# Performance work log

Measured on AMD Instinct MI355X. Metric: run time of the kernel, lower is better.

Reference implementation:

```python
import jax, jax.numpy as jnp
import numpy as np
from functools import partial

WIDTH = 2560
LRU = 2560
HEADS = 8
DCONV = 4
B = 4
L = 2048


def setup_inputs() -> dict:
    key = jax.random.key(0)
    ks = jax.random.split(key, 16)
    bw = LRU // HEADS
    x = jax.random.normal(ks[0], (B, L, WIDTH), dtype=jnp.float32)
    segment_pos = jnp.broadcast_to(jnp.arange(L, dtype=jnp.int32), (B, L))
    # indices of the last DCONV frames of the left-padded conv input (length L+DCONV-1)
    base = (jnp.arange(DCONV, dtype=jnp.int32) + (L - 1))
    conv_idx = jnp.broadcast_to(base, (B, LRU, DCONV))
    s = 0.02
    return {
        "x": x,
        "segment_pos": segment_pos,
        "conv_idx": conv_idx,
        "Wx": jax.random.normal(ks[1], (LRU, WIDTH), jnp.float32) * s,
        "bx": jax.random.normal(ks[2], (LRU,), jnp.float32) * s,
        "Wy": jax.random.normal(ks[3], (LRU, WIDTH), jnp.float32) * s,
        "conv_w": jax.random.normal(ks[4], (LRU, DCONV), jnp.float32) * s,  # depthwise kernel
        "conv_b": jax.random.normal(ks[5], (LRU,), jnp.float32) * s,
        "gx_w": jax.random.normal(ks[6], (HEADS, bw, bw), jnp.float32) * s,
        "gx_b": jax.random.normal(ks[7], (HEADS, bw), jnp.float32) * s,
        "ga_w": jax.random.normal(ks[8], (HEADS, bw, bw), jnp.float32) * s,
        "ga_b": jax.random.normal(ks[9], (HEADS, bw), jnp.float32) * s,
        "a_param": jax.random.normal(ks[10], (LRU,), jnp.float32),
        "y_bias": jax.random.normal(ks[11], (1, 1, LRU), jnp.float32) * s,
        "Wout": jax.random.normal(ks[12], (WIDTH, LRU), jnp.float32) * s,
        "bout": jax.random.normal(ks[13], (WIDTH,), jnp.float32) * s,
    }


def _block_diag(x, w):
    # x: [B,L,(h*i)], w: [h,i,j] -> [B,L,(h*j)]
    b, l, _ = x.shape
    h, bw, _ = w.shape
    xb = x.reshape(b, l, h, bw)
    y = jnp.einsum('blhi,hij->blhj', xb, w)
    return y.reshape(b, l, h * bw)


def _scan_op(c1, c2):
    a1, b1 = c1
    a2, b2 = c2
    return (a1 * a2, a2 * b1 + b2)


def reference(x, segment_pos, conv_idx, Wx, bx, Wy, conv_w, conv_b,
              gx_w, gx_b, ga_w, ga_b, a_param, y_bias, Wout, bout):
    dc = conv_w.shape[1]
    seqlen = x.shape[1]

    y = jnp.einsum('bld,ed->ble', x, Wy)                 # linear_y (no bias)
    xl = jnp.einsum('bld,ed->ble', x, Wx) + bx           # linear_x

    # causal depthwise conv1d, padding dc-1 on the left, keep first seqlen
    xpad = jnp.pad(xl, ((0, 0), (dc - 1, 0), (0, 0)))    # [B, L+dc-1, LRU]
    xc = conv_b + sum(conv_w[:, k] * xpad[:, k:k + seqlen, :] for k in range(dc))

    # conv_state: gather of padded (channels-first) input at conv_idx
    conv_state = jnp.take_along_axis(xpad.transpose(0, 2, 1), conv_idx.astype(jnp.int32), axis=2)

    gx = _block_diag(xc, gx_w)  # fuse_bias=True: bias added inside rg_lru
    ga = _block_diag(xc, ga_w)

    # rg_lru_ref
    reset = (segment_pos == 0).astype(x.dtype)[..., None]        # [B,L,1]
    gate_x = jax.nn.sigmoid(gx + gx_b.reshape(-1))
    gate_a = jax.nn.sigmoid(ga + ga_b.reshape(-1))
    c = -8.0 * jax.nn.softplus(a_param)
    log_a = c * gate_a
    a = jnp.exp(log_a) * (1.0 - reset)
    multiplier = jnp.sqrt(1.0 - jnp.exp(2.0 * log_a))
    multiplier = reset + (1.0 - reset) * multiplier
    normalized_x = xc * gate_x * multiplier

    _, h = jax.lax.associative_scan(_scan_op, (a, normalized_x), axis=1)
    last_h = h[:, -1]

    out = h * jax.nn.gelu(y + y_bias, approximate=False)
    out = jnp.einsum('ble,de->bld', out, Wout) + bout    # linear_out
    return out, conv_state, last_h
```

## Files before the change

### kernel.cpp

```cpp
#include <hip/hip_runtime.h>
#include <hip/hip_bf16.h>

#define WIDTH_ 2560
#define LRU_   2560
#define HEADS_ 8
#define BW_    320
#define DCONV_ 4
#define BB     4
#define LL     2048
#define MROWS  (BB*LL)
#define NCH    32
#define CLEN   (LL/NCH)

typedef unsigned short ushort_t;
typedef __attribute__((ext_vector_type(8))) short short8;
typedef __attribute__((ext_vector_type(4))) float f32x4;

__device__ __forceinline__ unsigned short f2bf(float f) {
  union { float f; unsigned u; } v; v.f = f;
  unsigned r = v.u + 0x7fffu + ((v.u >> 16) & 1u);
  return (unsigned short)(r >> 16);
}
__device__ __forceinline__ float bf2f(unsigned short h) {
  union { unsigned u; float f; } v; v.u = ((unsigned)h) << 16;
  return v.f;
}
__device__ __forceinline__ void async_load16(const void* g, void* l) {
  __builtin_amdgcn_global_load_lds(
      (const __attribute__((address_space(1))) unsigned*)g,
      (__attribute__((address_space(3))) unsigned*)l, 16, 0, 0);
}
__device__ __forceinline__ float sigmoidf_(float x) {
  return 1.f / (1.f + __expf(-x));
}
__device__ __forceinline__ size_t pkaddr(int e, int m, int PL) {
  return ((size_t)(e >> 3) * PL + m) * 8 + (e & 7);
}

__global__ void tp_pack(const float* __restrict__ src, ushort_t* __restrict__ dst,
                        int R, int C, int PL, int RO) {
  __shared__ float tile[64][65];
  const int r0 = blockIdx.x * 64, c0 = blockIdx.y * 64;
  const int t = threadIdx.x;
#pragma unroll
  for (int it = 0; it < 4; ++it) {
    int row = it * 16 + (t >> 4);
    int col = (t & 15) * 4;
    *(float4*)&tile[row][col] = *(const float4*)&src[(size_t)(r0 + row) * C + c0 + col];
  }
  __syncthreads();
#pragma unroll
  for (int it = 0; it < 2; ++it) {
    int c8 = it * 4 + (t >> 6);
    int m  = t & 63;
    ushort_t o[8];
#pragma unroll
    for (int j = 0; j < 8; ++j) o[j] = f2bf(tile[m][c8 * 8 + j]);
    *(short8*)&dst[((size_t)(c0 / 8 + c8) * PL + RO + r0 + m) * 8] = *(short8*)o;
  }
}

__global__ void gw_pack(const float* __restrict__ w, ushort_t* __restrict__ dst,
                        int RO, int n_) {
  int i = blockIdx.x * blockDim.x + threadIdx.x;
  if (i >= n_) return;
  int n = i % BW_;
  int k = (i / BW_) % BW_;
  int h = i / (BW_ * BW_);
  dst[((size_t)(h * 40 + (k >> 3)) * 640 + RO + n) * 8 + (k & 7)] =
      f2bf(w[((size_t)h * BW_ + k) * BW_ + n]);
}

__global__ void ctab_kernel(const float* __restrict__ apar, float* __restrict__ ctab) {
  int e = blockIdx.x * blockDim.x + threadIdx.x;
  if (e >= LRU_) return;
  float ap = apar[e];
  float sp = (ap > 15.f) ? ap : log1pf(expf(ap));
  ctab[e] = -8.f * sp;
}


#define STG_A(KT, H, BUF) do { \
  _Pragma("unroll") for (int u_ = 0; u_ < 2; ++u_) \
    async_load16(Ach + aoff[u_] + (size_t)(KT) * aKt + (H) * 2048, \
                 smem + ((BUF) * 2 + (H)) * 16384 + ldst[u_]); } while (0)
#define STG_B(KT, H, BUF) do { \
  _Pragma("unroll") for (int u_ = 0; u_ < 2; ++u_) \
    async_load16(Bch + boff[u_] + (size_t)(KT) * bKt + (H) * 2048, \
                 smem + 65536 + ((BUF) * 2 + (H)) * 16384 + ldst[u_]); } while (0)

#define PHASE(BUF, Q, STAGE_STMT, VMN) do { \
  __builtin_amdgcn_sched_barrier(0); \
  const char* Ah_ = smem + ((BUF) * 2 + wr) * 16384; \
  const char* Bh_ = smem + 65536 + ((BUF) * 2 + (wc >> 1)) * 16384; \
  if ((Q) == 0) { \
    _Pragma("unroll") for (int nf = 0; nf < 4; ++nf) \
      _Pragma("unroll") for (int s = 0; s < 2; ++s) \
        bfr[nf][s] = *(const short8*)(Bh_ + ((s * 4 + l4) * 128 + brow + nf * 16 + l15) * 16); \
  } \
  short8 a_[2][2]; \
  _Pragma("unroll") for (int mm = 0; mm < 2; ++mm) \
    _Pragma("unroll") for (int s = 0; s < 2; ++s) \
      a_[mm][s] = *(const short8*)(Ah_ + ((s * 4 + l4) * 128 + ((Q) * 2 + mm) * 16 + l15) * 16); \
  STAGE_STMT; \
  __builtin_amdgcn_sched_barrier(0); \
  __builtin_amdgcn_s_barrier(); \
  asm volatile("s_waitcnt lgkmcnt(0)" ::: "memory"); \
  __builtin_amdgcn_sched_barrier(0); \
  __builtin_amdgcn_s_setprio(1); \
  _Pragma("unroll") for (int mm = 0; mm < 2; ++mm) \
    _Pragma("unroll") for (int nf = 0; nf < 4; ++nf) \
      _Pragma("unroll") for (int s = 0; s < 2; ++s) \
        acc[(Q) * 2 + mm][nf] = __builtin_amdgcn_mfma_f32_16x16x32_bf16( \
            a_[mm][s], bfr[nf][s], acc[(Q) * 2 + mm][nf], 0, 0, 0); \
  __builtin_amdgcn_s_setprio(0); \
  if ((VMN) == 4)      asm volatile("s_waitcnt vmcnt(4)" ::: "memory"); \
  else if ((VMN) == 0) asm volatile("s_waitcnt vmcnt(0)" ::: "memory"); \
  __builtin_amdgcn_sched_barrier(0); \
  __builtin_amdgcn_s_barrier(); \
} while (0)

template<int EPI>
__global__ __launch_bounds__(512, 2)
void gemm_pk(const ushort_t* __restrict__ A,
             const ushort_t* __restrict__ B, int NPL,
             void* __restrict__ C0, void* __restrict__ C1,
             const float* __restrict__ bias) {
  __shared__ char smem[131072];
  const int tid = threadIdx.x;
  const int lane = tid & 63, w = tid >> 6;
  const int wr = w >> 2, wc = w & 3;
  const int l15 = lane & 15, l4 = lane >> 4;
  const int brow = (wc & 1) * 64;

  const int nblk = gridDim.x;
  const int TN = nblk >> 5;
  const int x8 = blockIdx.x & 7, c = blockIdx.x >> 3;
  const int tm = (x8 * 4 + c / TN) * 256;
  const int tn = (c % TN) * 256;

  const char* Ach = (const char*)A;
  const char* Bch = (const char*)B;
  const size_t aKt = (size_t)8 * MROWS * 16;
  const size_t bKt = (size_t)8 * NPL * 16;

  size_t aoff[2], boff[2]; int ldst[2];
#pragma unroll
  for (int u = 0; u < 2; ++u) {
    int lb = (u * 512 + tid) * 16;
    int slot = lb >> 11, m = (lb >> 4) & 127;
    aoff[u] = ((size_t)slot * MROWS + tm + m) * 16;
    boff[u] = ((size_t)slot * NPL + tn + m) * 16;
    ldst[u] = lb;
  }

  f32x4 acc[8][4] = {};
  short8 bfr[4][2];

  STG_B(0, 0, 0); STG_B(0, 1, 0); STG_A(0, 0, 0); STG_A(0, 1, 0);
  STG_B(1, 0, 1); STG_B(1, 1, 1);
  asm volatile("s_waitcnt vmcnt(4)" ::: "memory");
  __builtin_amdgcn_sched_barrier(0);
  __builtin_amdgcn_s_barrier();

#pragma unroll 1
  for (int i = 0; i < 20; ++i) {
    const int k1 = 2 * i + 1, k2 = 2 * i + 2, k3 = 2 * i + 3;
    const bool v2 = (k2 < 40), v3 = (k3 < 40);
    PHASE(0, 0, STG_A(k1, 0, 1), -1);
    PHASE(0, 1, STG_A(k1, 1, 1), -1);
    PHASE(0, 2, if (v2) STG_B(k2, 0, 0), -1);
    PHASE(0, 3, if (v2) STG_B(k2, 1, 0), (v2 ? 4 : 0));
    PHASE(1, 0, if (v2) STG_A(k2, 0, 0), -1);
    PHASE(1, 1, if (v2) STG_A(k2, 1, 0), -1);
    PHASE(1, 2, if (v3) STG_B(k3, 0, 1), -1);
    PHASE(1, 3, if (v3) STG_B(k3, 1, 1), (v3 ? 4 : (v2 ? 0 : -1)));
  }

  const int crow0 = tm + wr * 128 + l4 * 4;
  const int ccol0 = tn + wc * 64 + l15;
#pragma unroll
  for (int m = 0; m < 8; ++m)
#pragma unroll
    for (int n = 0; n < 4; ++n) {
      const int col = ccol0 + n * 16;
#pragma unroll
      for (int r = 0; r < 4; ++r) {
        const int row = crow0 + m * 16 + r;
        float v = acc[m][n][r];
        if (EPI == 0) {
          ((float*)C0)[(size_t)row * 2560 + col] = v + bias[col];
        } else {
          if (col < 2560)
            ((ushort_t*)C0)[pkaddr(col, row, MROWS)] = f2bf(v + bias[col]);
          else
            ((ushort_t*)C1)[pkaddr(col - 2560, row, MROWS)] = f2bf(v);
        }
      }
    }
}

__global__ __launch_bounds__(256, 2)
void gate_gemm(const ushort_t* __restrict__ A,
               const ushort_t* __restrict__ Bw,
               ushort_t* __restrict__ GX,
               ushort_t* __restrict__ AAo,
               const float* __restrict__ gxb, const float* __restrict__ gab,
               const float* __restrict__ ctab, const int* __restrict__ seg) {
  constexpr int BM = 128, NF = 2;
  __shared__ char smem[24576];
  const int tid = threadIdx.x;
  const int w = tid >> 6, lane = tid & 63;
  const int wr = w >> 1, wc = w & 1;
  const int l15 = lane & 15, l4 = lane >> 4;
  const int tm = blockIdx.x * BM;
  const int tn = blockIdx.y * 64;
  const int z = blockIdx.z;

  const char* aS[2]; int lda_[2];
#pragma unroll
  for (int u = 0; u < 2; ++u) {
    int lb = (u * 256 + tid) * 16;
    int slot = lb >> 11, m = (lb >> 4) & 127;
    aS[u] = (const char*)A + ((size_t)(z * 40 + slot) * MROWS + tm + m) * 16;
    lda_[u] = lb;
  }
  const char* bS; int ldb_;
  {
    int lb = tid * 16;
    int slot = lb >> 10, n = (lb >> 4) & 63;
    bS = (const char*)Bw + ((size_t)(z * 40 + slot) * 640 + tn + n) * 16;
    ldb_ = 8192 + lb;
  }
  const size_t aStep = (size_t)4 * MROWS * 16;
  const size_t bStep = (size_t)4 * 640 * 16;

#define GSTG(KT, BUF) do { \
  _Pragma("unroll") for (int u_ = 0; u_ < 2; ++u_) \
    async_load16(aS[u_] + (size_t)(KT) * aStep, smem + (BUF) * 12288 + lda_[u_]); \
  async_load16(bS + (size_t)(KT) * bStep, smem + (BUF) * 12288 + ldb_); \
} while (0)

  f32x4 acc[4][NF] = {};
  const int aRd = l4 * 2048 + (wr * 64 + l15) * 16;
  const int bRd = 8192 + l4 * 1024 + (wc * 32 + l15) * 16;

  GSTG(0, 0);
#pragma unroll 1
  for (int kt = 0; kt < 10; ++kt) {
    const int p = kt & 1;
    if (kt < 9) {
      GSTG(kt + 1, p ^ 1);
      asm volatile("s_waitcnt vmcnt(3)" ::: "memory");
    } else {
      asm volatile("s_waitcnt vmcnt(0)" ::: "memory");
    }
    __builtin_amdgcn_sched_barrier(0);
    __builtin_amdgcn_s_barrier();
    const char* buf = smem + p * 12288;
    short8 af[4], bfr[NF];
#pragma unroll
    for (int mf = 0; mf < 4; ++mf)
      af[mf] = *(const short8*)(buf + aRd + mf * 256);
#pragma unroll
    for (int nf = 0; nf < NF; ++nf)
      bfr[nf] = *(const short8*)(buf + bRd + nf * 256);
#pragma unroll
    for (int mf = 0; mf < 4; ++mf)
#pragma unroll
      for (int nf = 0; nf < NF; ++nf)
        acc[mf][nf] = __builtin_amdgcn_mfma_f32_16x16x32_bf16(af[mf], bfr[nf], acc[mf][nf], 0, 0, 0);
    __builtin_amdgcn_sched_barrier(0);
    __builtin_amdgcn_s_barrier();
  }
#undef GSTG

  const int crow0 = tm + wr * 64 + l4 * 4;
  const int ccol0 = tn + wc * 32 + l15;
#pragma unroll
  for (int mf = 0; mf < 4; ++mf) {
#pragma unroll
    for (int nf = 0; nf < NF; ++nf) {
      const int cih = ccol0 + nf * 16;
#pragma unroll
      for (int r = 0; r < 4; ++r) {
        const int row = crow0 + mf * 16 + r;
        if (cih < BW_) {
          const int gc = z * BW_ + cih;
          float v = acc[mf][nf][r] + gxb[gc];
          float xc = bf2f(A[pkaddr(gc, row, MROWS)]);
          GX[pkaddr(gc, row, MROWS)] = f2bf(xc * sigmoidf_(v));
        } else {
          const int gc = z * BW_ + cih - BW_;
          float v = acc[mf][nf][r] + gab[gc];
          float la = ctab[gc] * sigmoidf_(v);
          float av = (seg[row] == 0) ? 0.f : expf(la);
          AAo[pkaddr(gc, row, MROWS)] = f2bf(av);
        }
      }
    }
  }
}

__global__ void conv_pk(const ushort_t* __restrict__ xl, const float* __restrict__ convw,
                        const float* __restrict__ convb, ushort_t* __restrict__ xc) {
  int i = blockIdx.x * blockDim.x + threadIdx.x;
  if (i >= 320 * MROWS) return;
  int m = i % MROWS;
  int p = i / MROWS;
  int t = m % LL;
  const ushort_t* pl = xl + (size_t)p * MROWS * 8;
  short8 v0 = {}, v1 = {}, v2 = {}, v3;
  v3 = *(const short8*)(pl + (size_t)m * 8);
  if (t >= 1) v2 = *(const short8*)(pl + (size_t)(m - 1) * 8);
  if (t >= 2) v1 = *(const short8*)(pl + (size_t)(m - 2) * 8);
  if (t >= 3) v0 = *(const short8*)(pl + (size_t)(m - 3) * 8);
  ushort_t o[8];
#pragma unroll
  for (int u = 0; u < 8; ++u) {
    int e = p * 8 + u;
    float4 wv = ((const float4*)convw)[e];
    float acc = convb[e];
    acc += wv.x * bf2f((ushort_t)v0[u]);
    acc += wv.y * bf2f((ushort_t)v1[u]);
    acc += wv.z * bf2f((ushort_t)v2[u]);
    acc += wv.w * bf2f((ushort_t)v3[u]);
    o[u] = f2bf(acc);
  }
  *(short8*)(xc + (size_t)p * MROWS * 8 + (size_t)m * 8) = *(short8*)o;
}

__global__ void conv_state_kernel(const ushort_t* __restrict__ xl, const int* __restrict__ cidx,
                                  float* __restrict__ cs) {
  int i = blockIdx.x * blockDim.x + threadIdx.x;
  if (i >= BB * LRU_ * DCONV_) return;
  int e = (i / DCONV_) % LRU_;
  int b = i / (DCONV_ * LRU_);
  int idx = cidx[i];
  int ts = idx - (DCONV_ - 1);
  float v = 0.f;
  if (ts >= 0 && ts < LL) v = bf2f(xl[pkaddr(e, b * LL + ts, MROWS)]);
  cs[i] = v;
}

__global__ void scanA(const ushort_t* __restrict__ AA, const ushort_t* __restrict__ GX,
                      float* __restrict__ cA, float* __restrict__ cH) {
  int i = blockIdx.x * blockDim.x + threadIdx.x;
  if (i >= BB * NCH * LRU_) return;
  int e = i % LRU_;
  int c = (i / LRU_) % NCH;
  int b = i / (LRU_ * NCH);
  float Ap = 1.f, h = 0.f;
  size_t base = pkaddr(e, b * LL + c * CLEN, MROWS);
  for (int t = 0; t < CLEN; ++t) {
    size_t j = base + (size_t)t * 8;
    float a = bf2f(AA[j]);
    float nx = bf2f(GX[j]) * sqrtf(fmaxf(0.f, 1.f - a * a));
    Ap *= a;
    h = a * h + nx;
  }
  cA[i] = Ap; cH[i] = h;
}

__global__ void scanB(const float* __restrict__ cA, const float* __restrict__ cH,
                      float* __restrict__ hInit) {
  int i = blockIdx.x * blockDim.x + threadIdx.x;
  if (i >= BB * LRU_) return;
  int e = i % LRU_;
  int b = i / LRU_;
  float h = 0.f;
  for (int c = 0; c < NCH; ++c) {
    size_t j = ((size_t)b * NCH + c) * LRU_ + e;
    hInit[j] = h;
    h = cA[j] * h + cH[j];
  }
}

__global__ void scanC(const ushort_t* __restrict__ AA, const ushort_t* __restrict__ GXpre,
                      const float* __restrict__ hInit, const ushort_t* __restrict__ ybf,
                      const float* __restrict__ ybias, float* __restrict__ lastH) {
  int i = blockIdx.x * blockDim.x + threadIdx.x;
  if (i >= BB * NCH * LRU_) return;
  int e = i % LRU_;
  int c = (i / LRU_) % NCH;
  int b = i / (LRU_ * NCH);
  float h = hInit[i];
  float yb = ybias[e];
  ushort_t* pre = (ushort_t*)GXpre;
  size_t base = pkaddr(e, b * LL + c * CLEN, MROWS);
  for (int t = 0; t < CLEN; ++t) {
    size_t j = base + (size_t)t * 8;
    float a = bf2f(AA[j]);
    float nx = bf2f(GXpre[j]) * sqrtf(fmaxf(0.f, 1.f - a * a));
    h = a * h + nx;
    float yv = bf2f(ybf[j]) + yb;
    float g = 0.5f * yv * (1.f + erff(yv * 0.70710678118f));
    pre[j] = f2bf(h * g);
  }
  if (c == NCH - 1) lastH[(size_t)b * LRU_ + e] = h;
}

extern "C" void kernel_launch(void* const* d_in, const int* in_sizes, int n_in,
                              void* d_out, int out_size, void* d_ws, size_t ws_size,
                              hipStream_t stream) {
  const float* x     = (const float*)d_in[0];
  const int*   seg   = (const int*)d_in[1];
  const int*   cidx  = (const int*)d_in[2];
  const float* Wx    = (const float*)d_in[3];
  const float* bx    = (const float*)d_in[4];
  const float* Wy    = (const float*)d_in[5];
  const float* convw = (const float*)d_in[6];
  const float* convb = (const float*)d_in[7];
  const float* gxw   = (const float*)d_in[8];
  const float* gxb   = (const float*)d_in[9];
  const float* gaw   = (const float*)d_in[10];
  const float* gab   = (const float*)d_in[11];
  const float* apar  = (const float*)d_in[12];
  const float* ybias = (const float*)d_in[13];
  const float* Wout  = (const float*)d_in[14];
  const float* bout  = (const float*)d_in[15];

  float* out    = (float*)d_out;
  float* cs_out = out + (size_t)MROWS * WIDTH_;
  float* lh_out = cs_out + (size_t)BB * LRU_ * DCONV_;

  ushort_t* ybf = (ushort_t*)d_out;
  ushort_t* AA  = (ushort_t*)((char*)d_out + (size_t)41943040);

  const size_t SZ_BIG = (size_t)MROWS * LRU_ * 2;
  const size_t SZ_WC  = (size_t)(2 * LRU_) * WIDTH_ * 2;
  const size_t SZ_GW  = (size_t)HEADS_ * 640 * BW_ * 2;
  const size_t SZ_SM  = (size_t)BB * NCH * LRU_ * 4;
  size_t need = SZ_BIG * 3 + SZ_WC + SZ_GW + 10240 + SZ_SM * 3;
  if (ws_size < need) return;

  char* p = (char*)d_ws;
  ushort_t* xpk   = (ushort_t*)p; p += SZ_BIG;
  ushort_t* wpk   = (ushort_t*)p; p += SZ_WC;
  ushort_t* T2    = (ushort_t*)p; p += SZ_BIG;
  ushort_t* xcbf  = (ushort_t*)p; p += SZ_BIG;
  ushort_t* gwT   = (ushort_t*)p; p += SZ_GW;
  float*    ctab  = (float*)p;    p += 10240;
  float*    cA    = (float*)p;    p += SZ_SM;
  float*    cH    = (float*)p;    p += SZ_SM;
  float*    hInit = (float*)p;    p += SZ_SM;
  ushort_t* woutpk = wpk;

  const int BLK = 256;
  tp_pack<<<dim3(MROWS / 64, WIDTH_ / 64), 256, 0, stream>>>(x, xpk, MROWS, WIDTH_, MROWS, 0);
  tp_pack<<<dim3(LRU_ / 64, WIDTH_ / 64), 256, 0, stream>>>(Wx, wpk, LRU_, WIDTH_, 2 * LRU_, 0);
  tp_pack<<<dim3(LRU_ / 64, WIDTH_ / 64), 256, 0, stream>>>(Wy, wpk, LRU_, WIDTH_, 2 * LRU_, LRU_);

  gemm_pk<1><<<640, 512, 0, stream>>>(xpk, wpk, 2 * LRU_, T2, ybf, bx);

  tp_pack<<<dim3(LRU_ / 64, WIDTH_ / 64), 256, 0, stream>>>(Wout, woutpk, WIDTH_, LRU_, WIDTH_, 0);

  conv_pk<<<(320 * MROWS + BLK - 1) / BLK, BLK, 0, stream>>>(T2, convw, convb, xcbf);
  conv_state_kernel<<<(BB * LRU_ * DCONV_ + BLK - 1) / BLK, BLK, 0, stream>>>(T2, cidx, cs_out);

  gw_pack<<<(HEADS_ * BW_ * BW_ + BLK - 1) / BLK, BLK, 0, stream>>>(gxw, gwT, 0, HEADS_ * BW_ * BW_);
  gw_pack<<<(HEADS_ * BW_ * BW_ + BLK - 1) / BLK, BLK, 0, stream>>>(gaw, gwT, BW_, HEADS_ * BW_ * BW_);
  ctab_kernel<<<(LRU_ + BLK - 1) / BLK, BLK, 0, stream>>>(apar, ctab);

  gate_gemm<<<dim3(MROWS / 128, 10, HEADS_), BLK, 0, stream>>>(
      xcbf, gwT, T2, AA, gxb, gab, ctab, seg);

  scanA<<<(BB * NCH * LRU_ + BLK - 1) / BLK, BLK, 0, stream>>>(AA, T2, cA, cH);
  scanB<<<(BB * LRU_ + BLK - 1) / BLK, BLK, 0, stream>>>(cA, cH, hInit);
  scanC<<<(BB * NCH * LRU_ + BLK - 1) / BLK, BLK, 0, stream>>>(AA, T2, hInit, ybf, ybias, lh_out);

  gemm_pk<0><<<320, 512, 0, stream>>>(T2, woutpk, WIDTH_, out, nullptr, bout);
}
```

Before: 579.0 us.

## Keep full A row-tile resident in LDS for gate GEMM; fuse GELU into projection epilogue

The gate GEMM is restructured so each block loads its entire 128-row by 320-channel xc tile into LDS once and streams all 20 output column slices of the head's weights through a double buffer. Previously A was re-read for each of 10 column tiles, and xc was re-read from global memory in the epilogue. The GELU on y+bias moves into the first GEMM's epilogue, so the scan reads a precomputed gate and skips erf work inside the serial loop. The cost is 120KB of LDS per block, which lowers occupancy, along with a smaller grid of 512 blocks and erf evaluation in the GEMM epilogue.

Result: slower. 743.1 us (+28.3%).

```diff
diff --git a/kernel.cpp b/kernel.cpp
--- a/kernel.cpp
+++ b/kernel.cpp
@@ -125,7 +125,7 @@
 void gemm_pk(const ushort_t* __restrict__ A,
              const ushort_t* __restrict__ B, int NPL,
              void* __restrict__ C0, void* __restrict__ C1,
-             const float* __restrict__ bias) {
+             const float* __restrict__ bias, const float* __restrict__ ybias) {
   __shared__ char smem[131072];
   const int tid = threadIdx.x;
   const int lane = tid & 63, w = tid >> 6;
@@ -191,10 +191,13 @@
         if (EPI == 0) {
           ((float*)C0)[(size_t)row * 2560 + col] = v + bias[col];
         } else {
-          if (col < 2560)
+          if (col < 2560) {
             ((ushort_t*)C0)[pkaddr(col, row, MROWS)] = f2bf(v + bias[col]);
-          else
-            ((ushort_t*)C1)[pkaddr(col - 2560, row, MROWS)] = f2bf(v);
+          } else {
+            float yv = v + ybias[col - 2560];
+            float g = 0.5f * yv * (1.f + erff(yv * 0.70710678118f));
+            ((ushort_t*)C1)[pkaddr(col - 2560, row, MROWS)] = f2bf(g);
+          }
         }
       }
     }
@@ -207,99 +210,90 @@
                ushort_t* __restrict__ AAo,
                const float* __restrict__ gxb, const float* __restrict__ gab,
                const float* __restrict__ ctab, const int* __restrict__ seg) {
-  constexpr int BM = 128, NF = 2;
-  __shared__ char smem[24576];
+  __shared__ char smem[122880];
   const int tid = threadIdx.x;
-  const int w = tid >> 6, lane = tid & 63;
-  const int wr = w >> 1, wc = w & 1;
+  const int lane = tid & 63, w = tid >> 6;
   const int l15 = lane & 15, l4 = lane >> 4;
-  const int tm = blockIdx.x * BM;
-  const int tn = blockIdx.y * 64;
-  const int z = blockIdx.z;
-
-  const char* aS[2]; int lda_[2];
-#pragma unroll
-  for (int u = 0; u < 2; ++u) {
+  const int tm = blockIdx.x * 128;
+  const int z = blockIdx.y;
+
+#pragma unroll
+  for (int u = 0; u < 20; ++u) {
     int lb = (u * 256 + tid) * 16;
     int slot = lb >> 11, m = (lb >> 4) & 127;
-    aS[u] = (const char*)A + ((size_t)(z * 40 + slot) * MROWS + tm + m) * 16;
-    lda_[u] = lb;
-  }
-  const char* bS; int ldb_;
-  {
-    int lb = tid * 16;
-    int slot = lb >> 10, n = (lb >> 4) & 63;
-    bS = (const char*)Bw + ((size_t)(z * 40 + slot) * 640 + tn + n) * 16;
-    ldb_ = 8192 + lb;
-  }
-  const size_t aStep = (size_t)4 * MROWS * 16;
-  const size_t bStep = (size_t)4 * 640 * 16;
-
-#define GSTG(KT, BUF) do { \
-  _Pragma("unroll") for (int u_ = 0; u_ < 2; ++u_) \
-    async_load16(aS[u_] + (size_t)(KT) * aStep, smem + (BUF) * 12288 + lda_[u_]); \
-  async_load16(bS + (size_t)(KT) * bStep, smem + (BUF) * 12288 + ldb_); \
-} while (0)
-
-  f32x4 acc[4][NF] = {};
-  const int aRd = l4 * 2048 + (wr * 64 + l15) * 16;
-  const int bRd = 8192 + l4 * 1024 + (wc * 32 + l15) * 16;
-
-  GSTG(0, 0);
+    async_load16((const char*)A + ((size_t)(z * 40 + slot) * MROWS + tm + m) * 16,
+                 smem + lb);
+  }
+#define GSTG_B(S, BUF) do { \
+  _Pragma("unroll") for (int u_ = 0; u_ < 5; ++u_) { \
+    int lb_ = (u_ * 256 + tid) * 16; \
+    int slot_ = lb_ >> 9, n_ = (lb_ >> 4) & 31; \
+    async_load16((const char*)Bw + ((size_t)(z * 40 + slot_) * 640 + (S) * 32 + n_) * 16, \
+                 smem + 81920 + (BUF) * 20480 + lb_); \
+  } } while (0)
+
+  GSTG_B(0, 0);
+
 #pragma unroll 1
-  for (int kt = 0; kt < 10; ++kt) {
-    const int p = kt & 1;
-    if (kt < 9) {
-      GSTG(kt + 1, p ^ 1);
-      asm volatile("s_waitcnt vmcnt(3)" ::: "memory");
+  for (int s = 0; s < 20; ++s) {
+    const int p = s & 1;
+    if (s < 19) {
+      GSTG_B(s + 1, p ^ 1);
+      asm volatile("s_waitcnt vmcnt(5)" ::: "memory");
     } else {
       asm volatile("s_waitcnt vmcnt(0)" ::: "memory");
     }
     __builtin_amdgcn_sched_barrier(0);
     __builtin_amdgcn_s_barrier();
-    const char* buf = smem + p * 12288;
-    short8 af[4], bfr[NF];
-#pragma unroll
-    for (int mf = 0; mf < 4; ++mf)
-      af[mf] = *(const short8*)(buf + aRd + mf * 256);
-#pragma unroll
-    for (int nf = 0; nf < NF; ++nf)
-      bfr[nf] = *(const short8*)(buf + bRd + nf * 256);
-#pragma unroll
-    for (int mf = 0; mf < 4; ++mf)
-#pragma unroll
-      for (int nf = 0; nf < NF; ++nf)
-        acc[mf][nf] = __builtin_amdgcn_mfma_f32_16x16x32_bf16(af[mf], bfr[nf], acc[mf][nf], 0, 0, 0);
-    __builtin_amdgcn_sched_barrier(0);
-    __builtin_amdgcn_s_barrier();
-  }
-#undef GSTG
-
-  const int crow0 = tm + wr * 64 + l4 * 4;
-  const int ccol0 = tn + wc * 32 + l15;
-#pragma unroll
-  for (int mf = 0; mf < 4; ++mf) {
-#pragma unroll
-    for (int nf = 0; nf < NF; ++nf) {
-      const int cih = ccol0 + nf * 16;
-#pragma unroll
-      for (int r = 0; r < 4; ++r) {
-        const int row = crow0 + mf * 16 + r;
-        if (cih < BW_) {
-          const int gc = z * BW_ + cih;
-          float v = acc[mf][nf][r] + gxb[gc];
-          float xc = bf2f(A[pkaddr(gc, row, MROWS)]);
-          GX[pkaddr(gc, row, MROWS)] = f2bf(xc * sigmoidf_(v));
-        } else {
-          const int gc = z * BW_ + cih - BW_;
-          float v = acc[mf][nf][r] + gab[gc];
-          float la = ctab[gc] * sigmoidf_(v);
-          float av = (seg[row] == 0) ? 0.f : expf(la);
-          AAo[pkaddr(gc, row, MROWS)] = f2bf(av);
+
+    const char* Bb = smem + 81920 + p * 20480;
+    f32x4 acc[2][2] = {};
+#pragma unroll
+    for (int kk = 0; kk < 10; ++kk) {
+      short8 bfr[2], af[2];
+#pragma unroll
+      for (int nf = 0; nf < 2; ++nf)
+        bfr[nf] = *(const short8*)(Bb + (((kk * 4 + l4) * 32) + nf * 16 + l15) * 16);
+#pragma unroll
+      for (int mf = 0; mf < 2; ++mf)
+        af[mf] = *(const short8*)(smem + (((kk * 4 + l4) * 128) + w * 32 + mf * 16 + l15) * 16);
+#pragma unroll
+      for (int mf = 0; mf < 2; ++mf)
+#pragma unroll
+        for (int nf = 0; nf < 2; ++nf)
+          acc[mf][nf] = __builtin_amdgcn_mfma_f32_16x16x32_bf16(af[mf], bfr[nf], acc[mf][nf], 0, 0, 0);
+    }
+
+    const bool isGX = (s < 10);
+    const int cbase = (isGX ? s : s - 10) * 32;
+#pragma unroll
+    for (int mf = 0; mf < 2; ++mf) {
+#pragma unroll
+      for (int nf = 0; nf < 2; ++nf) {
+        const int cin = nf * 16 + l15;
+        const int gc = z * BW_ + cbase + cin;
+#pragma unroll
+        for (int r = 0; r < 4; ++r) {
+          const int lrow = w * 32 + mf * 16 + l4 * 4 + r;
+          const int row = tm + lrow;
+          if (isGX) {
+            float v = acc[mf][nf][r] + gxb[gc];
+            int slot = s * 4 + (cin >> 3);
+            float xc = bf2f(*(const ushort_t*)(smem + ((size_t)slot * 128 + lrow) * 16 + (cin & 7) * 2));
+            GX[pkaddr(gc, row, MROWS)] = f2bf(xc * sigmoidf_(v));
+          } else {
+            float v = acc[mf][nf][r] + gab[gc];
+            float la = ctab[gc] * sigmoidf_(v);
+            float av = (seg[row] == 0) ? 0.f : expf(la);
+            AAo[pkaddr(gc, row, MROWS)] = f2bf(av);
+          }
         }
       }
     }
-  }
+    __builtin_amdgcn_sched_barrier(0);
+    __builtin_amdgcn_s_barrier();
+  }
+#undef GSTG_B
 }
 
 __global__ void conv_pk(const ushort_t* __restrict__ xl, const float* __restrict__ convw,
@@ -377,15 +371,14 @@
 }
 
 __global__ void scanC(const ushort_t* __restrict__ AA, const ushort_t* __restrict__ GXpre,
-                      const float* __restrict__ hInit, const ushort_t* __restrict__ ybf,
-                      const float* __restrict__ ybias, float* __restrict__ lastH) {
+                      const float* __restrict__ hInit, const ushort_t* __restrict__ gbf,
+                      float* __restrict__ lastH) {
   int i = blockIdx.x * blockDim.x + threadIdx.x;
   if (i >= BB * NCH * LRU_) return;
   int e = i % LRU_;
   int c = (i / LRU_) % NCH;
   int b = i / (LRU_ * NCH);
   float h = hInit[i];
-  float yb = ybias[e];
   ushort_t* pre = (ushort_t*)GXpre;
   size_t base = pkaddr(e, b * LL + c * CLEN, MROWS);
   for (int t = 0; t < CLEN; ++t) {
@@ -393,8 +386,7 @@
     float a = bf2f(AA[j]);
     float nx = bf2f(GXpre[j]) * sqrtf(fmaxf(0.f, 1.f - a * a));
     h = a * h + nx;
-    float yv = bf2f(ybf[j]) + yb;
-    float g = 0.5f * yv * (1.f + erff(yv * 0.70710678118f));
+    float g = bf2f(gbf[j]);
     pre[j] = f2bf(h * g);
   }
   if (c == NCH - 1) lastH[(size_t)b * LRU_ + e] = h;
@@ -451,7 +443,7 @@
   tp_pack<<<dim3(LRU_ / 64, WIDTH_ / 64), 256, 0, stream>>>(Wx, wpk, LRU_, WIDTH_, 2 * LRU_, 0);
   tp_pack<<<dim3(LRU_ / 64, WIDTH_ / 64), 256, 0, stream>>>(Wy, wpk, LRU_, WIDTH_, 2 * LRU_, LRU_);
 
-  gemm_pk<1><<<640, 512, 0, stream>>>(xpk, wpk, 2 * LRU_, T2, ybf, bx);
+  gemm_pk<1><<<640, 512, 0, stream>>>(xpk, wpk, 2 * LRU_, T2, ybf, bx, ybias);
 
   tp_pack<<<dim3(LRU_ / 64, WIDTH_ / 64), 256, 0, stream>>>(Wout, woutpk, WIDTH_, LRU_, WIDTH_, 0);
 
@@ -462,12 +454,12 @@
   gw_pack<<<(HEADS_ * BW_ * BW_ + BLK - 1) / BLK, BLK, 0, stream>>>(gaw, gwT, BW_, HEADS_ * BW_ * BW_);
   ctab_kernel<<<(LRU_ + BLK - 1) / BLK, BLK, 0, stream>>>(apar, ctab);
 
-  gate_gemm<<<dim3(MROWS / 128, 10, HEADS_), BLK, 0, stream>>>(
+  gate_gemm<<<dim3(MROWS / 128, HEADS_), BLK, 0, stream>>>(
       xcbf, gwT, T2, AA, gxb, gab, ctab, seg);
 
   scanA<<<(BB * NCH * LRU_ + BLK - 1) / BLK, BLK, 0, stream>>>(AA, T2, cA, cH);
   scanB<<<(BB * LRU_ + BLK - 1) / BLK, BLK, 0, stream>>>(cA, cH, hInit);
-  scanC<<<(BB * NCH * LRU_ + BLK - 1) / BLK, BLK, 0, stream>>>(AA, T2, hInit, ybf, ybias, lh_out);
-
-  gemm_pk<0><<<320, 512, 0, stream>>>(T2, woutpk, WIDTH_, out, nullptr, bout);
-}
+  scanC<<<(BB * NCH * LRU_ + BLK - 1) / BLK, BLK, 0, stream>>>(AA, T2, hInit, ybf, lh_out);
+
+  gemm_pk<0><<<320, 512, 0, stream>>>(T2, woutpk, WIDTH_, out, nullptr, bout, nullptr);
+}
```
